# Kernel optimization log

Measured on AMD Instinct MI355X. Metric: run time of the kernel, lower is better.

Reference implementation:

```python
import jax, jax.numpy as jnp
import numpy as np

N_HEADS = 8
D_K = 64
NEG = 1e9


def setup_inputs() -> dict:
    key = jax.random.key(0)
    k1, k2, k3 = jax.random.split(key, 3)
    B, L, C = 4, 2048, 512
    x = jax.random.normal(k1, (B, L, C), dtype=jnp.float32)
    W_in = jax.random.normal(k2, (C, N_HEADS * D_K * 3), dtype=jnp.float32) * (C ** -0.5)
    b_in = jnp.zeros((N_HEADS * D_K * 3,), dtype=jnp.float32)
    W_out = jax.random.normal(k3, (N_HEADS * D_K, C), dtype=jnp.float32) * ((N_HEADS * D_K) ** -0.5)
    b_out = jnp.zeros((C,), dtype=jnp.float32)
    return {"x": x, "W_in": W_in, "b_in": b_in, "W_out": W_out, "b_out": b_out}


def reference(x, W_in, b_in, W_out, b_out):
    B, L, C = x.shape
    H, Dk = N_HEADS, D_K
    scale = Dk ** -0.5
    qkv = x @ W_in + b_in                       # [B, L, 3*H*Dk]
    qkv = qkv.reshape(B, L, H, 3 * Dk)
    q, k, v = jnp.split(qkv, 3, axis=-1)         # each [B, L, H, Dk]
    attn = jnp.einsum('bihd,bjhd->bijh', q, k) * scale  # [B, L, L, H]
    mask = jnp.tril(jnp.ones((L, L), dtype=x.dtype))[None, :, :, None]
    attn = attn * mask - NEG * (1.0 - mask)
    attn = jax.nn.softmax(attn, axis=2)          # softmax over j
    res = jnp.einsum('bijh,bjhd->bihd', attn, v)  # [B, L, H, Dk]
    res = res.reshape(B, L, H * Dk)
    res = res @ W_out + b_out
    return res + x
```

## Files before the change

### kernel.cpp

```cpp
#include <hip/hip_runtime.h>
#include <math.h>
#include <cstddef>


constexpr int B_SZ  = 4;
constexpr int L_SEQ = 2048;
constexpr int C_DIM = 512;
constexpr int H_N   = 8;
constexpr int DK    = 64;
constexpr int N_QKV = 1536;
constexpr int M_ROWS = B_SZ * L_SEQ;
constexpr float SCALE = 0.125f;
constexpr float DEFER_THR = 8.f;

typedef __attribute__((ext_vector_type(4))) float f32x4;
typedef __attribute__((ext_vector_type(8))) short bf16x8;

static __device__ inline ushort f2bf(float f) {
  unsigned u = __builtin_bit_cast(unsigned, f);
  u += 0x7fffu + ((u >> 16) & 1u);
  return (ushort)(u >> 16);
}

typedef __attribute__((address_space(1))) const unsigned int* gas1_t;
typedef __attribute__((address_space(3))) unsigned int* las3_t;
static __device__ inline void gload_lds16(const void* g, void* l) {
  __builtin_amdgcn_global_load_lds((gas1_t)g, (las3_t)l, 16, 0, 0);
}


__global__ __launch_bounds__(256) void prep_fused(
    const float* __restrict__ x, const float* __restrict__ W_in,
    const float* __restrict__ W_out, ushort* __restrict__ xbf,
    ushort* __restrict__ WinT, ushort* __restrict__ WoutT) {
  const int id = blockIdx.x;
  if (id < 4096) {
    const int i = id * 256 + threadIdx.x;
    const float4 v = reinterpret_cast<const float4*>(x)[i];
    ushort4 o;
    o.x = f2bf(v.x); o.y = f2bf(v.y); o.z = f2bf(v.z); o.w = f2bf(v.w);
    reinterpret_cast<ushort4*>(xbf)[i] = o;
    return;
  }
  __shared__ ushort T[64][65];
  const float* src;
  ushort* dst;
  int R, C, c0, r0;
  if (id < 4096 + 192) {
    const int t = id - 4096;
    src = W_in; dst = WinT; R = C_DIM; C = N_QKV;
    c0 = (t % 24) * 64; r0 = (t / 24) * 64;
  } else {
    const int t = id - 4288;
    src = W_out; dst = WoutT; R = C_DIM; C = C_DIM;
    c0 = (t % 8) * 64; r0 = (t / 8) * 64;
  }
#pragma unroll
  for (int p = 0; p < 16; ++p) {
    const int idx = threadIdx.x + p * 256;
    const int r = idx >> 6, c = idx & 63;
    T[r][c] = f2bf(src[(size_t)(r0 + r) * C + c0 + c]);
  }
  __syncthreads();
#pragma unroll
  for (int p = 0; p < 16; ++p) {
    const int idx = threadIdx.x + p * 256;
    const int r = idx >> 6, c = idx & 63;
    dst[(size_t)(c0 + r) * R + r0 + c] = T[c][r];
  }
}

template <int EPI>
__global__ __launch_bounds__(256) void gemm_bf16(
    const ushort* __restrict__ A, const ushort* __restrict__ Bt,
    const float* __restrict__ bias, ushort* __restrict__ Qo,
    ushort* __restrict__ Ko, ushort* __restrict__ Vto,
    float* __restrict__ outF, const float* __restrict__ resid,
    int N, int K) {
  __shared__ ushort Al[128 * 32];
  __shared__ ushort Bl[128 * 32];
  const int tid = threadIdx.x;
  const int w = tid >> 6, l = tid & 63;
  const int cc = l & 15, gg = l >> 4;
  const int bm = blockIdx.y * 128, bn = blockIdx.x * 128;
  const int wr = w >> 1, wc = w & 1;
  f32x4 acc[4][4] = {};

  for (int k0 = 0; k0 < K; k0 += 32) {
#pragma unroll
    for (int q = 0; q < 2; ++q) {
      const int cbase = q * 256 + w * 64;
      const int c = cbase + l;
      gload_lds16(A + (size_t)(bm + (c >> 2)) * K + k0 + (c & 3) * 8,
                  &Al[cbase * 8]);
      gload_lds16(Bt + (size_t)(bn + (c >> 2)) * K + k0 + (c & 3) * 8,
                  &Bl[cbase * 8]);
    }
    __syncthreads();
    bf16x8 aF[4], bF[4];
#pragma unroll
    for (int i = 0; i < 4; ++i)
      aF[i] = *reinterpret_cast<const bf16x8*>(
          &Al[(wr * 64 + i * 16 + cc) * 32 + gg * 8]);
#pragma unroll
    for (int j = 0; j < 4; ++j)
      bF[j] = *reinterpret_cast<const bf16x8*>(
          &Bl[(wc * 64 + j * 16 + cc) * 32 + gg * 8]);
#pragma unroll
    for (int i = 0; i < 4; ++i)
#pragma unroll
      for (int j = 0; j < 4; ++j)
        acc[i][j] = __builtin_amdgcn_mfma_f32_16x16x32_bf16(aF[i], bF[j],
                                                            acc[i][j], 0, 0, 0);
    __syncthreads();
  }

  if (EPI == 0) {
#pragma unroll
    for (int j = 0; j < 4; ++j) {
      const int colbase = bn + wc * 64 + j * 16;
      const int h = colbase / 192, rem = colbase % 192;
      const int type = rem / 64, d = (rem % 64) + cc;
      const float bv = bias[colbase + cc];
#pragma unroll
      for (int i = 0; i < 4; ++i) {
        const int rowbase = bm + wr * 64 + i * 16 + 4 * gg;
        const int b = rowbase >> 11, ll = rowbase & 2047;
        const size_t bh32 = (size_t)(b * H_N + h) * 32;
        if (type == 0) {
#pragma unroll
          for (int r = 0; r < 4; ++r)
            Qo[((size_t)(b * H_N + h) * L_SEQ + ll + r) * DK + d] =
                f2bf(acc[i][j][r] + bv);
        } else if (type == 1) {
#pragma unroll
          for (int r = 0; r < 4; ++r) {
            const int jg = ll + r;
            Ko[(bh32 + (jg >> 6)) * 4096 + (jg & 63) * 64 +
               (((d >> 3) ^ (jg & 7)) << 3) + (d & 7)] =
                f2bf(acc[i][j][r] + bv);
          }
        } else {
          ushort4 pk;
          pk.x = f2bf(acc[i][j][0] + bv);
          pk.y = f2bf(acc[i][j][1] + bv);
          pk.z = f2bf(acc[i][j][2] + bv);
          pk.w = f2bf(acc[i][j][3] + bv);
          const size_t idx = (bh32 + (ll >> 6)) * 4096 + (size_t)d * 64 +
                             ((((ll & 63) >> 3) ^ (d & 7)) << 3) + (ll & 7);
          *reinterpret_cast<ushort4*>(&Vto[idx]) = pk;
        }
      }
    }
  } else {
#pragma unroll
    for (int j = 0; j < 4; ++j) {
      const int col = bn + wc * 64 + j * 16 + cc;
      const float bv = bias[col];
#pragma unroll
      for (int i = 0; i < 4; ++i) {
        const int rowbase = bm + wr * 64 + i * 16 + 4 * gg;
#pragma unroll
        for (int r = 0; r < 4; ++r) {
          const size_t off = (size_t)(rowbase + r) * N + col;
          outF[off] = acc[i][j][r] + bv + resid[off];
        }
      }
    }
  }
}

#define STAGE(buf, tile)                                                     \
  {                                                                          \
    const ushort* kg_ = KoB + (size_t)(tile) * 4096 + w * 1024 + lane * 8;   \
    const ushort* vg_ = VtB + (size_t)(tile) * 4096 + w * 1024 + lane * 8;   \
    gload_lds16(kg_, &Ks[buf][w * 1024]);                                    \
    gload_lds16(kg_ + 512, &Ks[buf][w * 1024 + 512]);                        \
    gload_lds16(vg_, &Vs[buf][w * 1024]);                                    \
    gload_lds16(vg_ + 512, &Vs[buf][w * 1024 + 512]);                        \
  }

__global__ __launch_bounds__(256, 4) void attn_mfma(
    const ushort* __restrict__ Q, const ushort* __restrict__ Ko,
    const ushort* __restrict__ Vt, ushort* __restrict__ attn_out) {
  __shared__ ushort Ks[2][4096];
  __shared__ ushort Vs[2][4096];
  __shared__ ushort Pw_s[4][1024];
  const int id = blockIdx.x;
  const int bh = (id & 7) + 8 * ((id >> 3) & 3);
  const int qt = 31 - (id >> 5);
  const int tid = threadIdx.x;
  const int w = tid >> 6, lane = tid & 63;
  const int c = lane & 15, g = lane >> 4;
  const int b = bh >> 3, h = bh & 7;
  const ushort* KoB = Ko + (size_t)bh * 32 * 4096;
  const ushort* VtB = Vt + (size_t)bh * 32 * 4096;
  const int q0 = qt * 64 + w * 16;
  ushort* Pw = Pw_s[w];
  const int pc0 = (g ^ (c & 7)) * 8;
  const int pc1 = ((g + 4) ^ (c & 7)) * 8;

  bf16x8 qA[2];
  {
    const ushort* qp = Q + ((size_t)bh * L_SEQ + q0 + c) * DK + g * 8;
    qA[0] = *reinterpret_cast<const bf16x8*>(qp);
    qA[1] = *reinterpret_cast<const bf16x8*>(qp + 32);
  }

  f32x4 O[4] = {};
  float mrow[4] = {-INFINITY, -INFINITY, -INFINITY, -INFINITY};
  float lsum[4] = {};
  const f32x4 zero4 = {0.f, 0.f, 0.f, 0.f};

  STAGE(0, 0);
  __syncthreads();

  for (int jt = 0; jt <= qt; ++jt) {
    const int cur = jt & 1;
    if (jt < qt) STAGE(cur ^ 1, jt + 1);
    const ushort* Kc = Ks[cur];
    const ushort* Vc = Vs[cur];
    const int j0 = jt * 64;
    f32x4 S[4];
#pragma unroll
    for (int n = 0; n < 4; ++n) {
      const bf16x8 k0 = *reinterpret_cast<const bf16x8*>(&Kc[(n * 16 + c) * 64 + pc0]);
      const bf16x8 k1 = *reinterpret_cast<const bf16x8*>(&Kc[(n * 16 + c) * 64 + pc1]);
      S[n] = __builtin_amdgcn_mfma_f32_16x16x32_bf16(qA[0], k0, zero4, 0, 0, 0);
      S[n] = __builtin_amdgcn_mfma_f32_16x16x32_bf16(qA[1], k1, S[n], 0, 0, 0);
    }
    const bool diag = (jt == qt);
#pragma unroll
    for (int n = 0; n < 4; ++n)
#pragma unroll
      for (int r = 0; r < 4; ++r) {
        float v = S[n][r] * SCALE;
        if (diag && (j0 + n * 16 + c) > (q0 + 4 * g + r)) v = -INFINITY;
        S[n][r] = v;
      }
    float pm[4];
    int exceed = 0;
#pragma unroll
    for (int r = 0; r < 4; ++r) {
      pm[r] = fmaxf(fmaxf(S[0][r], S[1][r]), fmaxf(S[2][r], S[3][r]));
      exceed |= (pm[r] > mrow[r] + DEFER_THR);
    }
    if (__any(exceed)) {
#pragma unroll
      for (int r = 0; r < 4; ++r) {
        float fm = pm[r];
        fm = fmaxf(fm, __shfl_xor(fm, 1, 16));
        fm = fmaxf(fm, __shfl_xor(fm, 2, 16));
        fm = fmaxf(fm, __shfl_xor(fm, 4, 16));
        fm = fmaxf(fm, __shfl_xor(fm, 8, 16));
        const float mnew = fmaxf(mrow[r], fm);
        const float corr = __expf(mrow[r] - mnew);
        lsum[r] *= corr;
#pragma unroll
        for (int t = 0; t < 4; ++t) O[t][r] *= corr;
        mrow[r] = mnew;
      }
    }
#pragma unroll
    for (int n = 0; n < 4; ++n)
#pragma unroll
      for (int r = 0; r < 4; ++r) {
        const float p = __expf(S[n][r] - mrow[r]);
        S[n][r] = p;
        lsum[r] += p;
      }
#pragma unroll
    for (int n = 0; n < 4; ++n)
#pragma unroll
      for (int r = 0; r < 4; ++r) {
        const int row = 4 * g + r;
        Pw[row * 64 + ((2 * n + (c >> 3)) ^ (row & 7)) * 8 + (c & 7)] =
            f2bf(S[n][r]);
      }
    const bf16x8 pA0 = *reinterpret_cast<const bf16x8*>(&Pw[c * 64 + pc0]);
    const bf16x8 pA1 = *reinterpret_cast<const bf16x8*>(&Pw[c * 64 + pc1]);
#pragma unroll
    for (int t = 0; t < 4; ++t) {
      const bf16x8 v0 = *reinterpret_cast<const bf16x8*>(&Vc[(t * 16 + c) * 64 + pc0]);
      const bf16x8 v1 = *reinterpret_cast<const bf16x8*>(&Vc[(t * 16 + c) * 64 + pc1]);
      O[t] = __builtin_amdgcn_mfma_f32_16x16x32_bf16(pA0, v0, O[t], 0, 0, 0);
      O[t] = __builtin_amdgcn_mfma_f32_16x16x32_bf16(pA1, v1, O[t], 0, 0, 0);
    }
    __syncthreads();
  }
  float inv[4];
#pragma unroll
  for (int r = 0; r < 4; ++r) {
    float s = lsum[r];
    s += __shfl_xor(s, 1, 16);
    s += __shfl_xor(s, 2, 16);
    s += __shfl_xor(s, 4, 16);
    s += __shfl_xor(s, 8, 16);
    inv[r] = 1.f / s;
  }
#pragma unroll
  for (int t = 0; t < 4; ++t)
#pragma unroll
    for (int r = 0; r < 4; ++r)
      attn_out[((size_t)b * L_SEQ + q0 + 4 * g + r) * C_DIM + h * DK + t * 16 + c] =
          f2bf(O[t][r] * inv[r]);
}

extern "C" void kernel_launch(void* const* d_in, const int* in_sizes, int n_in,
                              void* d_out, int out_size, void* d_ws,
                              size_t ws_size, hipStream_t stream) {
  const float* x     = (const float*)d_in[0];
  const float* W_in  = (const float*)d_in[1];
  const float* b_in  = (const float*)d_in[2];
  const float* W_out = (const float*)d_in[3];
  const float* b_out = (const float*)d_in[4];
  float* out = (float*)d_out;

  ushort* xbf   = (ushort*)d_ws;
  ushort* WinT  = xbf + (size_t)M_ROWS * C_DIM;
  ushort* WoutT = WinT + (size_t)N_QKV * C_DIM;
  ushort* Qo    = WoutT + (size_t)C_DIM * C_DIM;
  ushort* Ko    = Qo + (size_t)M_ROWS * C_DIM;
  ushort* Vto   = Ko + (size_t)M_ROWS * C_DIM;
  ushort* attnb = Vto + (size_t)M_ROWS * C_DIM;

  prep_fused<<<dim3(4352, 1, 1), 256, 0, stream>>>(
      x, W_in, W_out, xbf, WinT, WoutT);
  gemm_bf16<0><<<dim3(N_QKV / 128, M_ROWS / 128), 256, 0, stream>>>(
      xbf, WinT, b_in, Qo, Ko, Vto, nullptr, nullptr, N_QKV, C_DIM);
  attn_mfma<<<dim3(1024, 1, 1), 256, 0, stream>>>(Qo, Ko, Vto, attnb);
  gemm_bf16<1><<<dim3(C_DIM / 128, M_ROWS / 128), 256, 0, stream>>>(
      attnb, WoutT, b_out, nullptr, nullptr, nullptr, out, x, C_DIM, C_DIM);
}
```

Baseline: 95.16 us.

## Process two 16-row query tiles per wave in attention, halving waves per block

Each wave in the attention kernel now handles 32 query rows, as two 16-row MFMA tiles, instead of 16. Blocks drop from 256 to 128 threads, and the K/V staging loop is rewritten so two waves still fill each 64x64 tile. Each K and V fragment read from LDS now feeds twice as many MFMAs, which cuts LDS traffic and staging per unit of compute. The cost is roughly double the accumulator and score registers per wave and fewer waves to hide latency, with launch bounds changed to (128, 2).

```diff
diff --git a/kernel.cpp b/kernel.cpp
--- a/kernel.cpp
+++ b/kernel.cpp
@@ -170,22 +170,23 @@
   }
 }
 
-#define STAGE(buf, tile)                                                     \
-  {                                                                          \
-    const ushort* kg_ = KoB + (size_t)(tile) * 4096 + w * 1024 + lane * 8;   \
-    const ushort* vg_ = VtB + (size_t)(tile) * 4096 + w * 1024 + lane * 8;   \
-    gload_lds16(kg_, &Ks[buf][w * 1024]);                                    \
-    gload_lds16(kg_ + 512, &Ks[buf][w * 1024 + 512]);                        \
-    gload_lds16(vg_, &Vs[buf][w * 1024]);                                    \
-    gload_lds16(vg_ + 512, &Vs[buf][w * 1024 + 512]);                        \
-  }
-
-__global__ __launch_bounds__(256, 4) void attn_mfma(
+#define STAGE(buf, tile)                                                   \
+  {                                                                        \
+    const ushort* kg_ = KoB + (size_t)(tile) * 4096 + w * 512 + lane * 8;  \
+    const ushort* vg_ = VtB + (size_t)(tile) * 4096 + w * 512 + lane * 8;  \
+    _Pragma("unroll")                                                      \
+    for (int r_ = 0; r_ < 4; ++r_) {                                       \
+      gload_lds16(kg_ + r_ * 1024, &Ks[buf][r_ * 1024 + w * 512]);         \
+      gload_lds16(vg_ + r_ * 1024, &Vs[buf][r_ * 1024 + w * 512]);         \
+    }                                                                      \
+  }
+
+__global__ __launch_bounds__(128, 2) void attn_mfma(
     const ushort* __restrict__ Q, const ushort* __restrict__ Ko,
     const ushort* __restrict__ Vt, ushort* __restrict__ attn_out) {
   __shared__ ushort Ks[2][4096];
   __shared__ ushort Vs[2][4096];
-  __shared__ ushort Pw_s[4][1024];
+  __shared__ ushort Pw_s[2][2][1024];
   const int id = blockIdx.x;
   const int bh = (id & 7) + 8 * ((id >> 3) & 3);
   const int qt = 31 - (id >> 5);
@@ -195,21 +196,25 @@
   const int b = bh >> 3, h = bh & 7;
   const ushort* KoB = Ko + (size_t)bh * 32 * 4096;
   const ushort* VtB = Vt + (size_t)bh * 32 * 4096;
-  const int q0 = qt * 64 + w * 16;
-  ushort* Pw = Pw_s[w];
+  const int q00 = qt * 64 + w * 32;
+  const int q01 = q00 + 16;
   const int pc0 = (g ^ (c & 7)) * 8;
   const int pc1 = ((g + 4) ^ (c & 7)) * 8;
 
-  bf16x8 qA[2];
+  bf16x8 qA0[2], qA1[2];
   {
-    const ushort* qp = Q + ((size_t)bh * L_SEQ + q0 + c) * DK + g * 8;
-    qA[0] = *reinterpret_cast<const bf16x8*>(qp);
-    qA[1] = *reinterpret_cast<const bf16x8*>(qp + 32);
-  }
-
-  f32x4 O[4] = {};
-  float mrow[4] = {-INFINITY, -INFINITY, -INFINITY, -INFINITY};
-  float lsum[4] = {};
+    const ushort* qp0 = Q + ((size_t)bh * L_SEQ + q00 + c) * DK + g * 8;
+    qA0[0] = *reinterpret_cast<const bf16x8*>(qp0);
+    qA0[1] = *reinterpret_cast<const bf16x8*>(qp0 + 32);
+    const ushort* qp1 = Q + ((size_t)bh * L_SEQ + q01 + c) * DK + g * 8;
+    qA1[0] = *reinterpret_cast<const bf16x8*>(qp1);
+    qA1[1] = *reinterpret_cast<const bf16x8*>(qp1 + 32);
+  }
+
+  f32x4 O0[4] = {}, O1[4] = {};
+  float m0[4] = {-INFINITY, -INFINITY, -INFINITY, -INFINITY};
+  float m1[4] = {-INFINITY, -INFINITY, -INFINITY, -INFINITY};
+  float ls0[4] = {}, ls1[4] = {};
   const f32x4 zero4 = {0.f, 0.f, 0.f, 0.f};
 
   STAGE(0, 0);
@@ -221,89 +226,129 @@
     const ushort* Kc = Ks[cur];
     const ushort* Vc = Vs[cur];
     const int j0 = jt * 64;
-    f32x4 S[4];
+    f32x4 S0[4], S1[4];
 #pragma unroll
     for (int n = 0; n < 4; ++n) {
       const bf16x8 k0 = *reinterpret_cast<const bf16x8*>(&Kc[(n * 16 + c) * 64 + pc0]);
       const bf16x8 k1 = *reinterpret_cast<const bf16x8*>(&Kc[(n * 16 + c) * 64 + pc1]);
-      S[n] = __builtin_amdgcn_mfma_f32_16x16x32_bf16(qA[0], k0, zero4, 0, 0, 0);
-      S[n] = __builtin_amdgcn_mfma_f32_16x16x32_bf16(qA[1], k1, S[n], 0, 0, 0);
+      S0[n] = __builtin_amdgcn_mfma_f32_16x16x32_bf16(qA0[0], k0, zero4, 0, 0, 0);
+      S0[n] = __builtin_amdgcn_mfma_f32_16x16x32_bf16(qA0[1], k1, S0[n], 0, 0, 0);
+      S1[n] = __builtin_amdgcn_mfma_f32_16x16x32_bf16(qA1[0], k0, zero4, 0, 0, 0);
+      S1[n] = __builtin_amdgcn_mfma_f32_16x16x32_bf16(qA1[1], k1, S1[n], 0, 0, 0);
     }
     const bool diag = (jt == qt);
 #pragma unroll
     for (int n = 0; n < 4; ++n)
 #pragma unroll
       for (int r = 0; r < 4; ++r) {
-        float v = S[n][r] * SCALE;
-        if (diag && (j0 + n * 16 + c) > (q0 + 4 * g + r)) v = -INFINITY;
-        S[n][r] = v;
-      }
-    float pm[4];
+        float v0 = S0[n][r] * SCALE;
+        float v1 = S1[n][r] * SCALE;
+        if (diag) {
+          const int jm = j0 + n * 16 + c;
+          if (jm > (q00 + 4 * g + r)) v0 = -INFINITY;
+          if (jm > (q01 + 4 * g + r)) v1 = -INFINITY;
+        }
+        S0[n][r] = v0;
+        S1[n][r] = v1;
+      }
+    float pm0[4], pm1[4];
     int exceed = 0;
 #pragma unroll
     for (int r = 0; r < 4; ++r) {
-      pm[r] = fmaxf(fmaxf(S[0][r], S[1][r]), fmaxf(S[2][r], S[3][r]));
-      exceed |= (pm[r] > mrow[r] + DEFER_THR);
+      pm0[r] = fmaxf(fmaxf(S0[0][r], S0[1][r]), fmaxf(S0[2][r], S0[3][r]));
+      pm1[r] = fmaxf(fmaxf(S1[0][r], S1[1][r]), fmaxf(S1[2][r], S1[3][r]));
+      exceed |= (pm0[r] > m0[r] + DEFER_THR) | (pm1[r] > m1[r] + DEFER_THR);
     }
     if (__any(exceed)) {
 #pragma unroll
       for (int r = 0; r < 4; ++r) {
-        float fm = pm[r];
+        float fm = pm0[r];
         fm = fmaxf(fm, __shfl_xor(fm, 1, 16));
         fm = fmaxf(fm, __shfl_xor(fm, 2, 16));
         fm = fmaxf(fm, __shfl_xor(fm, 4, 16));
         fm = fmaxf(fm, __shfl_xor(fm, 8, 16));
-        const float mnew = fmaxf(mrow[r], fm);
-        const float corr = __expf(mrow[r] - mnew);
-        lsum[r] *= corr;
-#pragma unroll
-        for (int t = 0; t < 4; ++t) O[t][r] *= corr;
-        mrow[r] = mnew;
+        const float mnew = fmaxf(m0[r], fm);
+        const float corr = __expf(m0[r] - mnew);
+        ls0[r] *= corr;
+#pragma unroll
+        for (int t = 0; t < 4; ++t) O0[t][r] *= corr;
+        m0[r] = mnew;
+      }
+#pragma unroll
+      for (int r = 0; r < 4; ++r) {
+        float fm = pm1[r];
+        fm = fmaxf(fm, __shfl_xor(fm, 1, 16));
+        fm = fmaxf(fm, __shfl_xor(fm, 2, 16));
+        fm = fmaxf(fm, __shfl_xor(fm, 4, 16));
+        fm = fmaxf(fm, __shfl_xor(fm, 8, 16));
+        const float mnew = fmaxf(m1[r], fm);
+        const float corr = __expf(m1[r] - mnew);
+        ls1[r] *= corr;
+#pragma unroll
+        for (int t = 0; t < 4; ++t) O1[t][r] *= corr;
+        m1[r] = mnew;
       }
     }
 #pragma unroll
     for (int n = 0; n < 4; ++n)
 #pragma unroll
       for (int r = 0; r < 4; ++r) {
-        const float p = __expf(S[n][r] - mrow[r]);
-        S[n][r] = p;
-        lsum[r] += p;
-      }
+        const float p0 = __expf(S0[n][r] - m0[r]);
+        const float p1 = __expf(S1[n][r] - m1[r]);
+        S0[n][r] = p0; ls0[r] += p0;
+        S1[n][r] = p1; ls1[r] += p1;
+      }
+    ushort* Pw0 = Pw_s[w][0];
+    ushort* Pw1 = Pw_s[w][1];
 #pragma unroll
     for (int n = 0; n < 4; ++n)
 #pragma unroll
       for (int r = 0; r < 4; ++r) {
         const int row = 4 * g + r;
-        Pw[row * 64 + ((2 * n + (c >> 3)) ^ (row & 7)) * 8 + (c & 7)] =
-            f2bf(S[n][r]);
-      }
-    const bf16x8 pA0 = *reinterpret_cast<const bf16x8*>(&Pw[c * 64 + pc0]);
-    const bf16x8 pA1 = *reinterpret_cast<const bf16x8*>(&Pw[c * 64 + pc1]);
+        const int off = row * 64 + ((2 * n + (c >> 3)) ^ (row & 7)) * 8 + (c & 7);
+        Pw0[off] = f2bf(S0[n][r]);
+        Pw1[off] = f2bf(S1[n][r]);
+      }
+    const bf16x8 pA00 = *reinterpret_cast<const bf16x8*>(&Pw0[c * 64 + pc0]);
+    const bf16x8 pA01 = *reinterpret_cast<const bf16x8*>(&Pw0[c * 64 + pc1]);
+    const bf16x8 pA10 = *reinterpret_cast<const bf16x8*>(&Pw1[c * 64 + pc0]);
+    const bf16x8 pA11 = *reinterpret_cast<const bf16x8*>(&Pw1[c * 64 + pc1]);
 #pragma unroll
     for (int t = 0; t < 4; ++t) {
       const bf16x8 v0 = *reinterpret_cast<const bf16x8*>(&Vc[(t * 16 + c) * 64 + pc0]);
       const bf16x8 v1 = *reinterpret_cast<const bf16x8*>(&Vc[(t * 16 + c) * 64 + pc1]);
-      O[t] = __builtin_amdgcn_mfma_f32_16x16x32_bf16(pA0, v0, O[t], 0, 0, 0);
-      O[t] = __builtin_amdgcn_mfma_f32_16x16x32_bf16(pA1, v1, O[t], 0, 0, 0);
+      O0[t] = __builtin_amdgcn_mfma_f32_16x16x32_bf16(pA00, v0, O0[t], 0, 0, 0);
+      O0[t] = __builtin_amdgcn_mfma_f32_16x16x32_bf16(pA01, v1, O0[t], 0, 0, 0);
+      O1[t] = __builtin_amdgcn_mfma_f32_16x16x32_bf16(pA10, v0, O1[t], 0, 0, 0);
+      O1[t] = __builtin_amdgcn_mfma_f32_16x16x32_bf16(pA11, v1, O1[t], 0, 0, 0);
     }
     __syncthreads();
   }
-  float inv[4];
+  float inv0[4], inv1[4];
 #pragma unroll
   for (int r = 0; r < 4; ++r) {
-    float s = lsum[r];
+    float s = ls0[r];
     s += __shfl_xor(s, 1, 16);
     s += __shfl_xor(s, 2, 16);
     s += __shfl_xor(s, 4, 16);
     s += __shfl_xor(s, 8, 16);
-    inv[r] = 1.f / s;
+    inv0[r] = 1.f / s;
+    float t = ls1[r];
+    t += __shfl_xor(t, 1, 16);
+    t += __shfl_xor(t, 2, 16);
+    t += __shfl_xor(t, 4, 16);
+    t += __shfl_xor(t, 8, 16);
+    inv1[r] = 1.f / t;
   }
 #pragma unroll
   for (int t = 0; t < 4; ++t)
 #pragma unroll
-    for (int r = 0; r < 4; ++r)
-      attn_out[((size_t)b * L_SEQ + q0 + 4 * g + r) * C_DIM + h * DK + t * 16 + c] =
-          f2bf(O[t][r] * inv[r]);
+    for (int r = 0; r < 4; ++r) {
+      attn_out[((size_t)b * L_SEQ + q00 + 4 * g + r) * C_DIM + h * DK + t * 16 + c] =
+          f2bf(O0[t][r] * inv0[r]);
+      attn_out[((size_t)b * L_SEQ + q01 + 4 * g + r) * C_DIM + h * DK + t * 16 + c] =
+          f2bf(O1[t][r] * inv1[r]);
+    }
 }
 
 extern "C" void kernel_launch(void* const* d_in, const int* in_sizes, int n_in,
@@ -328,7 +373,7 @@
       x, W_in, W_out, xbf, WinT, WoutT);
   gemm_bf16<0><<<dim3(N_QKV / 128, M_ROWS / 128), 256, 0, stream>>>(
       xbf, WinT, b_in, Qo, Ko, Vto, nullptr, nullptr, N_QKV, C_DIM);
-  attn_mfma<<<dim3(1024, 1, 1), 256, 0, stream>>>(Qo, Ko, Vto, attnb);
+  attn_mfma<<<dim3(1024, 1, 1), 128, 0, stream>>>(Qo, Ko, Vto, attnb);
   gemm_bf16<1><<<dim3(C_DIM / 128, M_ROWS / 128), 256, 0, stream>>>(
       attnb, WoutT, b_out, nullptr, nullptr, nullptr, out, x, C_DIM, C_DIM);
 }
```

New measurement: 109.8 us. +15.4%, slower.

## Load V directly from global into registers, drop V LDS staging

Applied to the files above, without the earlier changes.

Stores V as a plain transposed [bh, d, L] layout and has each wave load its V fragments straight from global memory into registers, issued before the softmax. This removes the V half of the LDS double buffer and raises the occupancy hint from 4 to 6 blocks per CU. The cost is that every wave re-reads the same V tile from global/L2, and the loads have no cross-iteration prefetch, so latency may be exposed.

```diff
diff --git a/kernel.cpp b/kernel.cpp
--- a/kernel.cpp
+++ b/kernel.cpp
@@ -146,9 +146,8 @@
           pk.y = f2bf(acc[i][j][1] + bv);
           pk.z = f2bf(acc[i][j][2] + bv);
           pk.w = f2bf(acc[i][j][3] + bv);
-          const size_t idx = (bh32 + (ll >> 6)) * 4096 + (size_t)d * 64 +
-                             ((((ll & 63) >> 3) ^ (d & 7)) << 3) + (ll & 7);
-          *reinterpret_cast<ushort4*>(&Vto[idx]) = pk;
+          *reinterpret_cast<ushort4*>(
+              &Vto[((size_t)(b * H_N + h) * DK + d) * L_SEQ + ll]) = pk;
         }
       }
     }
@@ -170,21 +169,17 @@
   }
 }
 
-#define STAGE(buf, tile)                                                     \
+#define STAGE_K(buf, tile)                                                   \
   {                                                                          \
     const ushort* kg_ = KoB + (size_t)(tile) * 4096 + w * 1024 + lane * 8;   \
-    const ushort* vg_ = VtB + (size_t)(tile) * 4096 + w * 1024 + lane * 8;   \
     gload_lds16(kg_, &Ks[buf][w * 1024]);                                    \
     gload_lds16(kg_ + 512, &Ks[buf][w * 1024 + 512]);                        \
-    gload_lds16(vg_, &Vs[buf][w * 1024]);                                    \
-    gload_lds16(vg_ + 512, &Vs[buf][w * 1024 + 512]);                        \
-  }
-
-__global__ __launch_bounds__(256, 4) void attn_mfma(
+  }
+
+__global__ __launch_bounds__(256, 6) void attn_mfma(
     const ushort* __restrict__ Q, const ushort* __restrict__ Ko,
     const ushort* __restrict__ Vt, ushort* __restrict__ attn_out) {
   __shared__ ushort Ks[2][4096];
-  __shared__ ushort Vs[2][4096];
   __shared__ ushort Pw_s[4][1024];
   const int id = blockIdx.x;
   const int bh = (id & 7) + 8 * ((id >> 3) & 3);
@@ -194,7 +189,7 @@
   const int c = lane & 15, g = lane >> 4;
   const int b = bh >> 3, h = bh & 7;
   const ushort* KoB = Ko + (size_t)bh * 32 * 4096;
-  const ushort* VtB = Vt + (size_t)bh * 32 * 4096;
+  const ushort* VtB = Vt + (size_t)bh * DK * L_SEQ;
   const int q0 = qt * 64 + w * 16;
   ushort* Pw = Pw_s[w];
   const int pc0 = (g ^ (c & 7)) * 8;
@@ -212,14 +207,13 @@
   float lsum[4] = {};
   const f32x4 zero4 = {0.f, 0.f, 0.f, 0.f};
 
-  STAGE(0, 0);
+  STAGE_K(0, 0);
   __syncthreads();
 
   for (int jt = 0; jt <= qt; ++jt) {
     const int cur = jt & 1;
-    if (jt < qt) STAGE(cur ^ 1, jt + 1);
+    if (jt < qt) STAGE_K(cur ^ 1, jt + 1);
     const ushort* Kc = Ks[cur];
-    const ushort* Vc = Vs[cur];
     const int j0 = jt * 64;
     f32x4 S[4];
 #pragma unroll
@@ -228,6 +222,13 @@
       const bf16x8 k1 = *reinterpret_cast<const bf16x8*>(&Kc[(n * 16 + c) * 64 + pc1]);
       S[n] = __builtin_amdgcn_mfma_f32_16x16x32_bf16(qA[0], k0, zero4, 0, 0, 0);
       S[n] = __builtin_amdgcn_mfma_f32_16x16x32_bf16(qA[1], k1, S[n], 0, 0, 0);
+    }
+    bf16x8 vb[4][2];
+#pragma unroll
+    for (int t = 0; t < 4; ++t) {
+      const ushort* vp = VtB + (size_t)(t * 16 + c) * L_SEQ + j0 + g * 8;
+      vb[t][0] = *reinterpret_cast<const bf16x8*>(vp);
+      vb[t][1] = *reinterpret_cast<const bf16x8*>(vp + 32);
     }
     const bool diag = (jt == qt);
 #pragma unroll
@@ -281,10 +282,8 @@
     const bf16x8 pA1 = *reinterpret_cast<const bf16x8*>(&Pw[c * 64 + pc1]);
 #pragma unroll
     for (int t = 0; t < 4; ++t) {
-      const bf16x8 v0 = *reinterpret_cast<const bf16x8*>(&Vc[(t * 16 + c) * 64 + pc0]);
-      const bf16x8 v1 = *reinterpret_cast<const bf16x8*>(&Vc[(t * 16 + c) * 64 + pc1]);
-      O[t] = __builtin_amdgcn_mfma_f32_16x16x32_bf16(pA0, v0, O[t], 0, 0, 0);
-      O[t] = __builtin_amdgcn_mfma_f32_16x16x32_bf16(pA1, v1, O[t], 0, 0, 0);
+      O[t] = __builtin_amdgcn_mfma_f32_16x16x32_bf16(pA0, vb[t][0], O[t], 0, 0, 0);
+      O[t] = __builtin_amdgcn_mfma_f32_16x16x32_bf16(pA1, vb[t][1], O[t], 0, 0, 0);
     }
     __syncthreads();
   }
```

New measurement: 168.4 us. +77.0%, slower.

## Fuse x fp32-to-bf16 conversion into QKV GEMM A-tile loads

Applied to the files above, without the earlier changes.

Drops the separate x-to-bf16 conversion pass and its workspace buffer. The QKV GEMM now loads fp32 A tiles directly into LDS with an XOR swizzle and converts them to bf16 in registers before the MFMA. This saves writing and re-reading an 8MB bf16 copy of x. In exchange, A-tile traffic per GEMM block doubles, because each of the 12 column blocks rereads fp32 x, and LDS use and conversion ALU work go up.

```diff
diff --git a/kernel.cpp b/kernel.cpp
--- a/kernel.cpp
+++ b/kernel.cpp
@@ -1,6 +1,8 @@
 #include <hip/hip_runtime.h>
+#include <hip/hip_bf16.h>
 #include <math.h>
 #include <cstddef>
+#include <cstring>
 
 
 constexpr int B_SZ  = 4;
@@ -15,6 +17,7 @@
 
 typedef __attribute__((ext_vector_type(4))) float f32x4;
 typedef __attribute__((ext_vector_type(8))) short bf16x8;
+typedef __attribute__((ext_vector_type(4))) unsigned int u32x4;
 
 static __device__ inline ushort f2bf(float f) {
   unsigned u = __builtin_bit_cast(unsigned, f);
@@ -22,6 +25,13 @@
   return (ushort)(u >> 16);
 }
 
+static __device__ inline unsigned pack_bf2(float a, float b) {
+  const __hip_bfloat162 v = __float22bfloat162_rn(make_float2(a, b));
+  unsigned u;
+  __builtin_memcpy(&u, &v, 4);
+  return u;
+}
+
 typedef __attribute__((address_space(1))) const unsigned int* gas1_t;
 typedef __attribute__((address_space(3))) unsigned int* las3_t;
 static __device__ inline void gload_lds16(const void* g, void* l) {
@@ -29,29 +39,19 @@
 }
 
 
-__global__ __launch_bounds__(256) void prep_fused(
-    const float* __restrict__ x, const float* __restrict__ W_in,
-    const float* __restrict__ W_out, ushort* __restrict__ xbf,
+__global__ __launch_bounds__(256) void prep_w(
+    const float* __restrict__ W_in, const float* __restrict__ W_out,
     ushort* __restrict__ WinT, ushort* __restrict__ WoutT) {
+  __shared__ ushort T[64][65];
   const int id = blockIdx.x;
-  if (id < 4096) {
-    const int i = id * 256 + threadIdx.x;
-    const float4 v = reinterpret_cast<const float4*>(x)[i];
-    ushort4 o;
-    o.x = f2bf(v.x); o.y = f2bf(v.y); o.z = f2bf(v.z); o.w = f2bf(v.w);
-    reinterpret_cast<ushort4*>(xbf)[i] = o;
-    return;
-  }
-  __shared__ ushort T[64][65];
   const float* src;
   ushort* dst;
   int R, C, c0, r0;
-  if (id < 4096 + 192) {
-    const int t = id - 4096;
+  if (id < 192) {
     src = W_in; dst = WinT; R = C_DIM; C = N_QKV;
-    c0 = (t % 24) * 64; r0 = (t / 24) * 64;
+    c0 = (id % 24) * 64; r0 = (id / 24) * 64;
   } else {
-    const int t = id - 4288;
+    const int t = id - 192;
     src = W_out; dst = WoutT; R = C_DIM; C = C_DIM;
     c0 = (t % 8) * 64; r0 = (t / 8) * 64;
   }
@@ -70,15 +70,19 @@
   }
 }
 
-template <int EPI>
+template <int EPI, bool AFP32>
 __global__ __launch_bounds__(256) void gemm_bf16(
-    const ushort* __restrict__ A, const ushort* __restrict__ Bt,
+    const void* __restrict__ Avoid, const ushort* __restrict__ Bt,
     const float* __restrict__ bias, ushort* __restrict__ Qo,
     ushort* __restrict__ Ko, ushort* __restrict__ Vto,
     float* __restrict__ outF, const float* __restrict__ resid,
     int N, int K) {
-  __shared__ ushort Al[128 * 32];
+  __shared__ char AlRaw[AFP32 ? 16384 : 8192];
   __shared__ ushort Bl[128 * 32];
+  float* Alf = reinterpret_cast<float*>(AlRaw);
+  ushort* Alh = reinterpret_cast<ushort*>(AlRaw);
+  const float* Af = (const float*)Avoid;
+  const ushort* Ah = (const ushort*)Avoid;
   const int tid = threadIdx.x;
   const int w = tid >> 6, l = tid & 63;
   const int cc = l & 15, gg = l >> 4;
@@ -87,21 +91,55 @@
   f32x4 acc[4][4] = {};
 
   for (int k0 = 0; k0 < K; k0 += 32) {
-#pragma unroll
-    for (int q = 0; q < 2; ++q) {
-      const int cbase = q * 256 + w * 64;
-      const int c = cbase + l;
-      gload_lds16(A + (size_t)(bm + (c >> 2)) * K + k0 + (c & 3) * 8,
-                  &Al[cbase * 8]);
-      gload_lds16(Bt + (size_t)(bn + (c >> 2)) * K + k0 + (c & 3) * 8,
-                  &Bl[cbase * 8]);
+    if (AFP32) {
+#pragma unroll
+      for (int q = 0; q < 4; ++q) {
+        const int cidx = q * 256 + tid;
+        const int row = cidx >> 3, lc = cidx & 7;
+        gload_lds16(Af + (size_t)(bm + row) * K + k0 + ((lc ^ (row & 7)) << 2),
+                    &Alf[(q * 256 + w * 64) * 4]);
+      }
+#pragma unroll
+      for (int q = 0; q < 2; ++q) {
+        const int cbase = q * 256 + w * 64;
+        const int c = cbase + l;
+        gload_lds16(Bt + (size_t)(bn + (c >> 2)) * K + k0 + (c & 3) * 8,
+                    &Bl[cbase * 8]);
+      }
+    } else {
+#pragma unroll
+      for (int q = 0; q < 2; ++q) {
+        const int cbase = q * 256 + w * 64;
+        const int c = cbase + l;
+        gload_lds16(Ah + (size_t)(bm + (c >> 2)) * K + k0 + (c & 3) * 8,
+                    &Alh[cbase * 8]);
+        gload_lds16(Bt + (size_t)(bn + (c >> 2)) * K + k0 + (c & 3) * 8,
+                    &Bl[cbase * 8]);
+      }
     }
     __syncthreads();
     bf16x8 aF[4], bF[4];
-#pragma unroll
-    for (int i = 0; i < 4; ++i)
-      aF[i] = *reinterpret_cast<const bf16x8*>(
-          &Al[(wr * 64 + i * 16 + cc) * 32 + gg * 8]);
+    if (AFP32) {
+#pragma unroll
+      for (int i = 0; i < 4; ++i) {
+        const int rowA = wr * 64 + i * 16 + cc;
+        const float4 fa = *reinterpret_cast<const float4*>(
+            &Alf[rowA * 32 + (((2 * gg) ^ (cc & 7)) << 2)]);
+        const float4 fb = *reinterpret_cast<const float4*>(
+            &Alf[rowA * 32 + (((2 * gg + 1) ^ (cc & 7)) << 2)]);
+        u32x4 up;
+        up[0] = pack_bf2(fa.x, fa.y);
+        up[1] = pack_bf2(fa.z, fa.w);
+        up[2] = pack_bf2(fb.x, fb.y);
+        up[3] = pack_bf2(fb.z, fb.w);
+        aF[i] = __builtin_bit_cast(bf16x8, up);
+      }
+    } else {
+#pragma unroll
+      for (int i = 0; i < 4; ++i)
+        aF[i] = *reinterpret_cast<const bf16x8*>(
+            &Alh[(wr * 64 + i * 16 + cc) * 32 + gg * 8]);
+    }
 #pragma unroll
     for (int j = 0; j < 4; ++j)
       bF[j] = *reinterpret_cast<const bf16x8*>(
@@ -316,19 +354,17 @@
   const float* b_out = (const float*)d_in[4];
   float* out = (float*)d_out;
 
-  ushort* xbf   = (ushort*)d_ws;
-  ushort* WinT  = xbf + (size_t)M_ROWS * C_DIM;
+  ushort* WinT  = (ushort*)d_ws;
   ushort* WoutT = WinT + (size_t)N_QKV * C_DIM;
   ushort* Qo    = WoutT + (size_t)C_DIM * C_DIM;
   ushort* Ko    = Qo + (size_t)M_ROWS * C_DIM;
   ushort* Vto   = Ko + (size_t)M_ROWS * C_DIM;
   ushort* attnb = Vto + (size_t)M_ROWS * C_DIM;
 
-  prep_fused<<<dim3(4352, 1, 1), 256, 0, stream>>>(
-      x, W_in, W_out, xbf, WinT, WoutT);
-  gemm_bf16<0><<<dim3(N_QKV / 128, M_ROWS / 128), 256, 0, stream>>>(
-      xbf, WinT, b_in, Qo, Ko, Vto, nullptr, nullptr, N_QKV, C_DIM);
+  prep_w<<<dim3(256, 1, 1), 256, 0, stream>>>(W_in, W_out, WinT, WoutT);
+  gemm_bf16<0, true><<<dim3(N_QKV / 128, M_ROWS / 128), 256, 0, stream>>>(
+      x, WinT, b_in, Qo, Ko, Vto, nullptr, nullptr, N_QKV, C_DIM);
   attn_mfma<<<dim3(1024, 1, 1), 256, 0, stream>>>(Qo, Ko, Vto, attnb);
-  gemm_bf16<1><<<dim3(C_DIM / 128, M_ROWS / 128), 256, 0, stream>>>(
+  gemm_bf16<1, false><<<dim3(C_DIM / 128, M_ROWS / 128), 256, 0, stream>>>(
       attnb, WoutT, b_out, nullptr, nullptr, nullptr, out, x, C_DIM, C_DIM);
 }
```

New measurement: 95.43 us. Within noise of the previous version (+0.3%).
